# Kernel optimization log

Measured on AMD Instinct MI355X. Metric: run time of the kernel, lower is better.

The kernel has to match this reference:

```python
import jax, jax.numpy as jnp
import numpy as np

C = 128   # d_pair, fixed by the fp8 tri-mul kernel assert
H = 128   # d_hidden


def layer_norm(x, w, b, eps=1e-5):
    m = jnp.mean(x, axis=-1, keepdims=True)
    v = jnp.mean(jnp.square(x - m), axis=-1, keepdims=True)
    return (x - m) * jax.lax.rsqrt(v + eps) * w + b


def setup_inputs() -> dict:
    key = jax.random.key(0)
    ks = jax.random.split(key, 12)
    B, N = 1, 512
    s_in = 1.0 / np.sqrt(C)
    s_h = 1.0 / np.sqrt(H)
    return {
        "z": jax.random.normal(ks[0], (B, N, N, C), jnp.float32),
        "mask": jnp.ones((B, N, N), jnp.float32),
        "ln_in_w": jnp.ones((C,), jnp.float32),
        "ln_in_b": jnp.zeros((C,), jnp.float32),
        "w_ap": jax.random.normal(ks[1], (C, H), jnp.float32) * s_in,
        "b_ap": jnp.zeros((H,), jnp.float32),
        "w_ag": jax.random.normal(ks[2], (C, H), jnp.float32) * s_in,
        "b_ag": jnp.zeros((H,), jnp.float32),
        "w_bp": jax.random.normal(ks[3], (C, H), jnp.float32) * s_in,
        "b_bp": jnp.zeros((H,), jnp.float32),
        "w_bg": jax.random.normal(ks[4], (C, H), jnp.float32) * s_in,
        "b_bg": jnp.zeros((H,), jnp.float32),
        "ln_out_w": jnp.ones((H,), jnp.float32),
        "ln_out_b": jnp.zeros((H,), jnp.float32),
        "w_o": jax.random.normal(ks[5], (H, C), jnp.float32) * s_h,
        "b_o": jnp.zeros((C,), jnp.float32),
        "w_g": jax.random.normal(ks[6], (C, C), jnp.float32) * s_in,
        "b_g": jnp.zeros((C,), jnp.float32),
    }


def reference(z, mask, ln_in_w, ln_in_b, w_ap, b_ap, w_ag, b_ag,
              w_bp, b_bp, w_bg, b_bg, ln_out_w, ln_out_b, w_o, b_o, w_g, b_g):
    # Triangular multiplicative update (outgoing), gated projections.
    z_ln = layer_norm(z, ln_in_w, ln_in_b)                      # [B,N,N,C]
    m = mask[..., None]                                         # [B,N,N,1]
    a = m * jax.nn.sigmoid(z_ln @ w_ag + b_ag) * (z_ln @ w_ap + b_ap)
    b = m * jax.nn.sigmoid(z_ln @ w_bg + b_bg) * (z_ln @ w_bp + b_bp)
    # outgoing: x[b,i,j,c] = sum_k a[b,i,k,c] * b[b,j,k,c]
    x = jnp.einsum("bikc,bjkc->bijc", a, b)                     # [B,N,N,H]
    x = layer_norm(x, ln_out_w, ln_out_b)
    g = jax.nn.sigmoid(z_ln @ w_g + b_g)                        # output gate
    return g * (x @ w_o + b_o)
```

## Files before the change

kernel.cpp:

```cpp
#include <hip/hip_runtime.h>
#include <hip/hip_bf16.h>
#include <stdint.h>

#define NDIM 512
#define NN (NDIM*NDIM)
#define CDIM 128
#define LDSP 136

typedef __attribute__((ext_vector_type(8))) short short8;
typedef __attribute__((ext_vector_type(4))) short short4v;
typedef __attribute__((ext_vector_type(4))) float f32x4;
typedef unsigned long long ull;

__device__ __forceinline__ unsigned short f2bf(float f) {
    union { float f; uint32_t u; } v; v.f = f;
    uint32_t u = v.u;
    return (unsigned short)((u + 0x7FFFu + ((u >> 16) & 1u)) >> 16);
}
__device__ __forceinline__ float bf2f(unsigned short b) {
    union { uint32_t u; float f; } v; v.u = ((uint32_t)b) << 16;
    return v.f;
}
__device__ __forceinline__ f32x4 mfma16(short8 a, short8 b, f32x4 c) {
    return __builtin_amdgcn_mfma_f32_16x16x32_bf16(a, b, c, 0, 0, 0);
}
__device__ __forceinline__ void gl_lds16(const void* g, void* l) {
    __builtin_amdgcn_global_load_lds((const __attribute__((address_space(1))) void*)g,
                                     (__attribute__((address_space(3))) void*)l,
                                     16, 0, 0);
}

__global__ void k0_prep(const float* __restrict__ w_ag, const float* __restrict__ w_ap,
                        const float* __restrict__ w_bg, const float* __restrict__ w_bp,
                        const float* __restrict__ w_g,  const float* __restrict__ w_o,
                        unsigned short* __restrict__ Wfrag, unsigned short* __restrict__ Wo_t)
{
    int idx = blockIdx.x * 256 + threadIdx.x;
    if (idx < 10240) {
        int lane = idx & 63;
        int n  = (idx >> 6) & 3;
        int kk = (idx >> 8) & 3;
        int h  = (idx >> 10) & 1;
        int s  = idx >> 11;
        const float* w = (s==0) ? w_ag : (s==1) ? w_ap : (s==2) ? w_bg : (s==3) ? w_bp : w_g;
        int col = h*64 + n*16 + (lane & 15);
        int k0  = kk*32 + (lane >> 4)*8;
        short8 pk;
        #pragma unroll
        for (int e = 0; e < 8; e++)
            pk[e] = (short)f2bf(w[(k0 + e)*128 + col]);
        *(short8*)(Wfrag + (size_t)idx*8) = pk;
    } else if (idx < 10240 + 16384) {
        int i2 = idx - 10240;
        int cc = i2 >> 7, hh = i2 & 127;
        Wo_t[i2] = f2bf(w_o[hh*128 + cc]);
    }
}

__global__ __launch_bounds__(256, 2) void k1_proj(
    const float* __restrict__ z, const float* __restrict__ mask,
    const float* __restrict__ lnw, const float* __restrict__ lnb,
    const unsigned short* __restrict__ Wfrag,
    const float* __restrict__ b_ag, const float* __restrict__ b_ap,
    const float* __restrict__ b_bg, const float* __restrict__ b_bp,
    const float* __restrict__ b_g,
    unsigned short* __restrict__ a_t, unsigned short* __restrict__ b_t,
    unsigned short* __restrict__ g_out)
{
    __shared__ unsigned short zb[128*LDSP];
    __shared__ float mask_s[128];
    __shared__ float lnw_s[128];
    __shared__ float lnb_s[128];
    __shared__ float bias_s[640];

    const int t = threadIdx.x;
    const int pos0 = blockIdx.x * 128;
    const int tid2 = t >> 1, half = t & 1;
    const int wave = t >> 6, lane = t & 63;
    const int lr = lane & 15, lh = lane >> 4;

    if (t < 128) {
        lnw_s[t] = lnw[t];
        lnb_s[t] = lnb[t];
        mask_s[t] = mask[pos0 + t];
    }
    for (int i = t; i < 640; i += 256) {
        int s = i >> 7, c = i & 127;
        const float* bp = (s==0) ? b_ag : (s==1) ? b_ap : (s==2) ? b_bg : (s==3) ? b_bp : b_g;
        bias_s[i] = bp[c];
    }

    float v[64];
    float s0 = 0.f, s1 = 0.f;
    {
        const float* zr = z + (size_t)(pos0 + tid2) * CDIM + half * 64;
        #pragma unroll
        for (int i = 0; i < 16; i++) {
            float4 q = *(const float4*)(zr + i*4);
            v[i*4+0] = q.x; v[i*4+1] = q.y; v[i*4+2] = q.z; v[i*4+3] = q.w;
        }
        #pragma unroll
        for (int i = 0; i < 64; i++) { s0 += v[i]; s1 += v[i]*v[i]; }
        s0 += __shfl_xor(s0, 1);
        s1 += __shfl_xor(s1, 1);
    }
    __syncthreads();
    {
        float m  = s0 * (1.f/128.f);
        float va = s1 * (1.f/128.f) - m*m;
        float rs = rsqrtf(va + 1e-5f);
        #pragma unroll
        for (int i = 0; i < 8; i++) {
            short8 pk;
            #pragma unroll
            for (int j = 0; j < 8; j++) {
                int c = half*64 + i*8 + j;
                pk[j] = (short)f2bf((v[i*8+j]-m)*rs*lnw_s[c] + lnb_s[c]);
            }
            *(short8*)&zb[tid2*LDSP + half*64 + i*8] = pk;
        }
    }
    __syncthreads();

    const int rowA0 = (wave*32 + lr)*LDSP;
    const int rowA1 = (wave*32 + 16 + lr)*LDSP;
    const unsigned short* wfl = Wfrag + (size_t)lane*8;

    auto gemmh = [&](int s, int h, f32x4 (&acc)[2][4]) {
        const unsigned short* wf = wfl + (size_t)(s*2 + h)*8192;
        short8 wbuf[16];
        #pragma unroll
        for (int i = 0; i < 16; i++)
            wbuf[i] = *(const short8*)(wf + i*512);
        #pragma unroll
        for (int m = 0; m < 2; m++)
            #pragma unroll
            for (int n = 0; n < 4; n++) { f32x4 zz = {0.f,0.f,0.f,0.f}; acc[m][n] = zz; }
        #pragma unroll
        for (int kk = 0; kk < 4; kk++) {
            const int k0 = kk*32 + lh*8;
            short8 af0 = *(const short8*)&zb[rowA0 + k0];
            short8 af1 = *(const short8*)&zb[rowA1 + k0];
            #pragma unroll
            for (int n = 0; n < 4; n++) {
                acc[0][n] = mfma16(af0, wbuf[kk*4 + n], acc[0][n]);
                acc[1][n] = mfma16(af1, wbuf[kk*4 + n], acc[1][n]);
            }
        }
    };

    auto pair_half = [&](int sG, int sP, int h, unsigned short* dstg) {
        f32x4 G[2][4], P[2][4];
        gemmh(sG, h, G);
        gemmh(sP, h, P);
        const int odd = lh & 1;
        const int base = wave*32 + lh*4 + (odd ? 12 : 0);
        #pragma unroll
        for (int n = 0; n < 4; n++) {
            int col = h*64 + n*16 + lr;
            float bgv = bias_s[sG*128 + col];
            float bpv = bias_s[sP*128 + col];
            union { short4v v; ull u; } p0, p1;
            #pragma unroll
            for (int r = 0; r < 4; r++) {
                float g0 = 1.f / (1.f + __expf(-(G[0][n][r] + bgv)));
                p0.v[r] = (short)f2bf(mask_s[wave*32 + lh*4 + r] * g0 * (P[0][n][r] + bpv));
                float g1 = 1.f / (1.f + __expf(-(G[1][n][r] + bgv)));
                p1.v[r] = (short)f2bf(mask_s[wave*32 + 16 + lh*4 + r] * g1 * (P[1][n][r] + bpv));
            }
            ull r0 = __shfl_xor(p0.u, 16);
            ull r1 = __shfl_xor(p1.u, 16);
            union { ull u[2]; short8 v; } outv;
            outv.u[0] = odd ? r1 : p0.u;
            outv.u[1] = odd ? p1.u : r0;
            *(short8*)(dstg + (size_t)col*NN + pos0 + base) = outv.v;
        }
    };

    pair_half(0, 1, 0, a_t);
    pair_half(0, 1, 1, a_t);
    pair_half(2, 3, 0, b_t);
    pair_half(2, 3, 1, b_t);

    f32x4 G0[2][4], G1[2][4];
    gemmh(4, 0, G0);
    gemmh(4, 1, G1);
    __syncthreads();
    #pragma unroll
    for (int m = 0; m < 2; m++) {
        int rb = wave*32 + m*16 + lh*4;
        #pragma unroll
        for (int n = 0; n < 4; n++) {
            int c0 = n*16 + lr;
            int c1 = 64 + n*16 + lr;
            float b0 = bias_s[512 + c0];
            float b1 = bias_s[512 + c1];
            #pragma unroll
            for (int r = 0; r < 4; r++) {
                zb[(rb + r)*LDSP + c0] = f2bf(1.f / (1.f + __expf(-(G0[m][n][r] + b0))));
                zb[(rb + r)*LDSP + c1] = f2bf(1.f / (1.f + __expf(-(G1[m][n][r] + b1))));
            }
        }
    }
    __syncthreads();
    {
        const unsigned short* src = zb + tid2*LDSP + half*64;
        unsigned short* dst = g_out + (size_t)(pos0 + tid2)*CDIM + half*64;
        #pragma unroll
        for (int i = 0; i < 8; i++)
            *(short8*)(dst + i*8) = *(const short8*)(src + i*8);
    }
}

__global__ __launch_bounds__(256, 2) void k2_einsum(
    const unsigned short* __restrict__ a_t,
    const unsigned short* __restrict__ b_t,
    unsigned short* __restrict__ x_t)
{
    __shared__ unsigned short As[128*64];
    __shared__ unsigned short Bs[128*64];

    const int c  = blockIdx.y;
    const int ti = (blockIdx.x >> 2) * 128;
    const int tj = (blockIdx.x & 3) * 128;
    const int t = threadIdx.x;
    const int wave = t >> 6, lane = t & 63;
    const int lr = lane & 15, lh = lane >> 4;
    const int wm = wave >> 1, wn = wave & 1;

    const unsigned short* Ag = a_t + (size_t)c*NN + (size_t)ti*NDIM;
    const unsigned short* Bg = b_t + (size_t)c*NN + (size_t)tj*NDIM;

    const int srow = wave*32 + (lane >> 3);
    const int scol = (lane & 7) * 8;

    f32x4 acc[4][4] = {};

    for (int k0 = 0; k0 < NDIM; k0 += 64) {
        __syncthreads();
        #pragma unroll
        for (int it = 0; it < 4; it++) {
            int r = srow + it*8;
            gl_lds16(Ag + (size_t)r*NDIM + k0 + scol, (void*)(As + (wave*32 + it*8)*64));
            gl_lds16(Bg + (size_t)r*NDIM + k0 + scol, (void*)(Bs + (wave*32 + it*8)*64));
        }
        asm volatile("s_waitcnt vmcnt(0)" ::: "memory");
        __syncthreads();
        #pragma unroll
        for (int kk = 0; kk < 2; kk++) {
            const int kof = kk*32 + lh*8;
            short8 af[4], bfr[4];
            #pragma unroll
            for (int m = 0; m < 4; m++)
                af[m] = *(const short8*)&As[(wm*64 + m*16 + lr)*64 + kof];
            #pragma unroll
            for (int n = 0; n < 4; n++)
                bfr[n] = *(const short8*)&Bs[(wn*64 + n*16 + lr)*64 + kof];
            #pragma unroll
            for (int m = 0; m < 4; m++)
                #pragma unroll
                for (int n = 0; n < 4; n++)
                    acc[m][n] = mfma16(af[m], bfr[n], acc[m][n]);
        }
    }

    #pragma unroll
    for (int m = 0; m < 4; m++) {
        int row = ti + wm*64 + m*16 + lh*4;
        #pragma unroll
        for (int n = 0; n < 4; n++) {
            int col = tj + wn*64 + n*16 + lr;
            unsigned short* dst = x_t + (size_t)c*NN + (size_t)row*NDIM + col;
            #pragma unroll
            for (int r = 0; r < 4; r++)
                dst[(size_t)r*NDIM] = f2bf(acc[m][n][r]);
        }
    }
}

__global__ __launch_bounds__(256, 2) void k3_out(
    const unsigned short* __restrict__ x_t,
    const unsigned short* __restrict__ g_in,
    const unsigned short* __restrict__ Wo_t,
    const float* __restrict__ lnw, const float* __restrict__ lnb,
    const float* __restrict__ b_o,
    float* __restrict__ out)
{
    __shared__ unsigned short xb[128*LDSP];
    __shared__ unsigned short zl[128*LDSP];
    __shared__ float lnw_s[128];
    __shared__ float lnb_s[128];
    __shared__ float bo_s[128];

    const int t = threadIdx.x;
    const int pos0 = blockIdx.x * 128;
    const int tid2 = t >> 1, half = t & 1;
    const int wave = t >> 6, lane = t & 63;
    const int lr = lane & 15, lh = lane >> 4;

    if (t < 128) { lnw_s[t] = lnw[t]; lnb_s[t] = lnb[t]; bo_s[t] = b_o[t]; }

    {
        const unsigned short* src = x_t + (size_t)tid2*NN + pos0 + half*64;
        unsigned short* dst = xb + tid2*LDSP + half*64;
        #pragma unroll
        for (int i = 0; i < 8; i++)
            *(short8*)(dst + i*8) = *(const short8*)(src + i*8);
    }
    __syncthreads();

    {
        float v[64];
        float s0 = 0.f, s1 = 0.f;
        #pragma unroll
        for (int i = 0; i < 64; i++) {
            float x = bf2f(xb[(half*64 + i)*LDSP + tid2]);
            v[i] = x; s0 += x; s1 += x*x;
        }
        s0 += __shfl_xor(s0, 1);
        s1 += __shfl_xor(s1, 1);
        float m  = s0 * (1.f/128.f);
        float va = s1 * (1.f/128.f) - m*m;
        float rs = rsqrtf(va + 1e-5f);
        #pragma unroll
        for (int i = 0; i < 64; i++) {
            int cc = half*64 + i;
            zl[tid2*LDSP + cc] = f2bf((v[i]-m)*rs*lnw_s[cc] + lnb_s[cc]);
        }
    }
    __syncthreads();

    {
        const unsigned short* src = Wo_t + ((size_t)tid2*128 + half*64);
        unsigned short* dst = xb + tid2*LDSP + half*64;
        #pragma unroll
        for (int i = 0; i < 8; i++)
            *(short8*)(dst + i*8) = *(const short8*)(src + i*8);
    }
    __syncthreads();

    f32x4 acc[2][8];
    #pragma unroll
    for (int m = 0; m < 2; m++)
        #pragma unroll
        for (int n = 0; n < 8; n++) { f32x4 zz = {0.f,0.f,0.f,0.f}; acc[m][n] = zz; }

    #pragma unroll
    for (int kk = 0; kk < 4; kk++) {
        const int k0 = kk*32 + lh*8;
        short8 af0 = *(const short8*)&zl[(wave*32 + lr)*LDSP + k0];
        short8 af1 = *(const short8*)&zl[(wave*32 + 16 + lr)*LDSP + k0];
        #pragma unroll
        for (int n = 0; n < 8; n++) {
            short8 bf = *(const short8*)&xb[(n*16 + lr)*LDSP + k0];
            acc[0][n] = mfma16(af0, bf, acc[0][n]);
            acc[1][n] = mfma16(af1, bf, acc[1][n]);
        }
    }
    __syncthreads();

    {
        const unsigned short* src = g_in + (size_t)(pos0 + tid2)*CDIM + half*64;
        unsigned short* dst = zl + tid2*LDSP + half*64;
        #pragma unroll
        for (int i = 0; i < 8; i++)
            *(short8*)(dst + i*8) = *(const short8*)(src + i*8);
    }
    __syncthreads();

    #pragma unroll
    for (int m = 0; m < 2; m++) {
        int rb = wave*32 + m*16 + lh*4;
        #pragma unroll
        for (int n = 0; n < 8; n++) {
            int col = n*16 + lr;
            float bo = bo_s[col];
            #pragma unroll
            for (int r = 0; r < 4; r++) {
                int row = rb + r;
                float gv = bf2f(zl[row*LDSP + col]);
                out[(size_t)(pos0 + row)*CDIM + col] = gv * (acc[m][n][r] + bo);
            }
        }
    }
}

extern "C" void kernel_launch(void* const* d_in, const int* in_sizes, int n_in,
                              void* d_out, int out_size, void* d_ws, size_t ws_size,
                              hipStream_t stream) {
    const float* z        = (const float*)d_in[0];
    const float* mask     = (const float*)d_in[1];
    const float* ln_in_w  = (const float*)d_in[2];
    const float* ln_in_b  = (const float*)d_in[3];
    const float* w_ap     = (const float*)d_in[4];
    const float* b_ap     = (const float*)d_in[5];
    const float* w_ag     = (const float*)d_in[6];
    const float* b_ag     = (const float*)d_in[7];
    const float* w_bp     = (const float*)d_in[8];
    const float* b_bp     = (const float*)d_in[9];
    const float* w_bg     = (const float*)d_in[10];
    const float* b_bg     = (const float*)d_in[11];
    const float* ln_out_w = (const float*)d_in[12];
    const float* ln_out_b = (const float*)d_in[13];
    const float* w_o      = (const float*)d_in[14];
    const float* b_o      = (const float*)d_in[15];
    const float* w_g      = (const float*)d_in[16];
    const float* b_g      = (const float*)d_in[17];

    char* ws = (char*)d_ws;
    const size_t BUF = (size_t)NN * 128 * 2;
    unsigned short* a_t   = (unsigned short*)(ws);
    unsigned short* b_t   = (unsigned short*)(ws + BUF);
    unsigned short* g_b   = (unsigned short*)(ws + 2*BUF);
    unsigned short* x_t   = (unsigned short*)(ws + 3*BUF);
    unsigned short* Wfrag = (unsigned short*)(ws + 4*BUF);
    unsigned short* Wo_t  = (unsigned short*)(ws + 4*BUF + (size_t)10240*8*2);

    k0_prep<<<104, 256, 0, stream>>>(w_ag, w_ap, w_bg, w_bp, w_g, w_o, Wfrag, Wo_t);
    k1_proj<<<NN/128, 256, 0, stream>>>(z, mask, ln_in_w, ln_in_b, Wfrag,
                                        b_ag, b_ap, b_bg, b_bp, b_g, a_t, b_t, g_b);
    k2_einsum<<<dim3(16, 128), 256, 0, stream>>>(a_t, b_t, x_t);
    k3_out<<<NN/128, 256, 0, stream>>>(x_t, g_b, Wo_t, ln_out_w, ln_out_b, b_o,
                                       (float*)d_out);
}
```

Baseline: 307.4 us.

## Switch intermediates to fp16 and split k1 projections across 8 waves

```diff
diff --git a/kernel.cpp b/kernel.cpp
--- a/kernel.cpp
+++ b/kernel.cpp
@@ -10,19 +10,22 @@
 typedef __attribute__((ext_vector_type(8))) short short8;
 typedef __attribute__((ext_vector_type(4))) short short4v;
 typedef __attribute__((ext_vector_type(4))) float f32x4;
+typedef __attribute__((ext_vector_type(8))) _Float16 half8;
 typedef unsigned long long ull;
 
-__device__ __forceinline__ unsigned short f2bf(float f) {
-    union { float f; uint32_t u; } v; v.f = f;
-    uint32_t u = v.u;
-    return (unsigned short)((u + 0x7FFFu + ((u >> 16) & 1u)) >> 16);
-}
-__device__ __forceinline__ float bf2f(unsigned short b) {
-    union { uint32_t u; float f; } v; v.u = ((uint32_t)b) << 16;
-    return v.f;
+__device__ __forceinline__ unsigned short f2h(float f) {
+    union { _Float16 h; unsigned short u; } v;
+    v.h = (_Float16)f;
+    return v.u;
+}
+__device__ __forceinline__ float h2f(unsigned short u) {
+    union { _Float16 h; unsigned short u; } v;
+    v.u = u;
+    return (float)v.h;
 }
 __device__ __forceinline__ f32x4 mfma16(short8 a, short8 b, f32x4 c) {
-    return __builtin_amdgcn_mfma_f32_16x16x32_bf16(a, b, c, 0, 0, 0);
+    return __builtin_amdgcn_mfma_f32_16x16x32_f16(
+        __builtin_bit_cast(half8, a), __builtin_bit_cast(half8, b), c, 0, 0, 0);
 }
 __device__ __forceinline__ void gl_lds16(const void* g, void* l) {
     __builtin_amdgcn_global_load_lds((const __attribute__((address_space(1))) void*)g,
@@ -48,16 +51,16 @@
         short8 pk;
         #pragma unroll
         for (int e = 0; e < 8; e++)
-            pk[e] = (short)f2bf(w[(k0 + e)*128 + col]);
+            pk[e] = (short)f2h(w[(k0 + e)*128 + col]);
         *(short8*)(Wfrag + (size_t)idx*8) = pk;
     } else if (idx < 10240 + 16384) {
         int i2 = idx - 10240;
         int cc = i2 >> 7, hh = i2 & 127;
-        Wo_t[i2] = f2bf(w_o[hh*128 + cc]);
-    }
-}
-
-__global__ __launch_bounds__(256, 2) void k1_proj(
+        Wo_t[i2] = f2h(w_o[hh*128 + cc]);
+    }
+}
+
+__global__ __launch_bounds__(512, 4) void k1_proj(
     const float* __restrict__ z, const float* __restrict__ mask,
     const float* __restrict__ lnw, const float* __restrict__ lnb,
     const unsigned short* __restrict__ Wfrag,
@@ -75,8 +78,9 @@
 
     const int t = threadIdx.x;
     const int pos0 = blockIdx.x * 128;
-    const int tid2 = t >> 1, half = t & 1;
+    const int row4 = t >> 2, q = t & 3;
     const int wave = t >> 6, lane = t & 63;
+    const int wl = wave & 3, wg = wave >> 2;
     const int lr = lane & 15, lh = lane >> 4;
 
     if (t < 128) {
@@ -84,25 +88,27 @@
         lnb_s[t] = lnb[t];
         mask_s[t] = mask[pos0 + t];
     }
-    for (int i = t; i < 640; i += 256) {
+    for (int i = t; i < 640; i += 512) {
         int s = i >> 7, c = i & 127;
         const float* bp = (s==0) ? b_ag : (s==1) ? b_ap : (s==2) ? b_bg : (s==3) ? b_bp : b_g;
         bias_s[i] = bp[c];
     }
 
-    float v[64];
+    float v[32];
     float s0 = 0.f, s1 = 0.f;
     {
-        const float* zr = z + (size_t)(pos0 + tid2) * CDIM + half * 64;
-        #pragma unroll
-        for (int i = 0; i < 16; i++) {
-            float4 q = *(const float4*)(zr + i*4);
-            v[i*4+0] = q.x; v[i*4+1] = q.y; v[i*4+2] = q.z; v[i*4+3] = q.w;
-        }
-        #pragma unroll
-        for (int i = 0; i < 64; i++) { s0 += v[i]; s1 += v[i]*v[i]; }
+        const float* zr = z + (size_t)(pos0 + row4) * CDIM + q * 32;
+        #pragma unroll
+        for (int i = 0; i < 8; i++) {
+            float4 qv = *(const float4*)(zr + i*4);
+            v[i*4+0] = qv.x; v[i*4+1] = qv.y; v[i*4+2] = qv.z; v[i*4+3] = qv.w;
+        }
+        #pragma unroll
+        for (int i = 0; i < 32; i++) { s0 += v[i]; s1 += v[i]*v[i]; }
         s0 += __shfl_xor(s0, 1);
         s1 += __shfl_xor(s1, 1);
+        s0 += __shfl_xor(s0, 2);
+        s1 += __shfl_xor(s1, 2);
     }
     __syncthreads();
     {
@@ -110,20 +116,20 @@
         float va = s1 * (1.f/128.f) - m*m;
         float rs = rsqrtf(va + 1e-5f);
         #pragma unroll
-        for (int i = 0; i < 8; i++) {
+        for (int i = 0; i < 4; i++) {
             short8 pk;
             #pragma unroll
             for (int j = 0; j < 8; j++) {
-                int c = half*64 + i*8 + j;
-                pk[j] = (short)f2bf((v[i*8+j]-m)*rs*lnw_s[c] + lnb_s[c]);
+                int c = q*32 + i*8 + j;
+                pk[j] = (short)f2h((v[i*8+j]-m)*rs*lnw_s[c] + lnb_s[c]);
             }
-            *(short8*)&zb[tid2*LDSP + half*64 + i*8] = pk;
-        }
-    }
-    __syncthreads();
-
-    const int rowA0 = (wave*32 + lr)*LDSP;
-    const int rowA1 = (wave*32 + 16 + lr)*LDSP;
+            *(short8*)&zb[row4*LDSP + q*32 + i*8] = pk;
+        }
+    }
+    __syncthreads();
+
+    const int rowA0 = (wl*32 + lr)*LDSP;
+    const int rowA1 = (wl*32 + 16 + lr)*LDSP;
     const unsigned short* wfl = Wfrag + (size_t)lane*8;
 
     auto gemmh = [&](int s, int h, f32x4 (&acc)[2][4]) {
@@ -154,7 +160,7 @@
         gemmh(sG, h, G);
         gemmh(sP, h, P);
         const int odd = lh & 1;
-        const int base = wave*32 + lh*4 + (odd ? 12 : 0);
+        const int base = wl*32 + lh*4 + (odd ? 12 : 0);
         #pragma unroll
         for (int n = 0; n < 4; n++) {
             int col = h*64 + n*16 + lr;
@@ -164,9 +170,9 @@
             #pragma unroll
             for (int r = 0; r < 4; r++) {
                 float g0 = 1.f / (1.f + __expf(-(G[0][n][r] + bgv)));
-                p0.v[r] = (short)f2bf(mask_s[wave*32 + lh*4 + r] * g0 * (P[0][n][r] + bpv));
+                p0.v[r] = (short)f2h(mask_s[wl*32 + lh*4 + r] * g0 * (P[0][n][r] + bpv));
                 float g1 = 1.f / (1.f + __expf(-(G[1][n][r] + bgv)));
-                p1.v[r] = (short)f2bf(mask_s[wave*32 + 16 + lh*4 + r] * g1 * (P[1][n][r] + bpv));
+                p1.v[r] = (short)f2h(mask_s[wl*32 + 16 + lh*4 + r] * g1 * (P[1][n][r] + bpv));
             }
             ull r0 = __shfl_xor(p0.u, 16);
             ull r1 = __shfl_xor(p1.u, 16);
@@ -177,37 +183,35 @@
         }
     };
 
-    pair_half(0, 1, 0, a_t);
-    pair_half(0, 1, 1, a_t);
-    pair_half(2, 3, 0, b_t);
-    pair_half(2, 3, 1, b_t);
-
-    f32x4 G0[2][4], G1[2][4];
-    gemmh(4, 0, G0);
-    gemmh(4, 1, G1);
+    if (wg == 0) {
+        pair_half(0, 1, 0, a_t);
+        pair_half(0, 1, 1, a_t);
+    } else {
+        pair_half(2, 3, 0, b_t);
+        pair_half(2, 3, 1, b_t);
+    }
+
+    f32x4 G[2][4];
+    gemmh(4, wg, G);
     __syncthreads();
     #pragma unroll
     for (int m = 0; m < 2; m++) {
-        int rb = wave*32 + m*16 + lh*4;
+        int rb = wl*32 + m*16 + lh*4;
         #pragma unroll
         for (int n = 0; n < 4; n++) {
-            int c0 = n*16 + lr;
-            int c1 = 64 + n*16 + lr;
+            int c0 = wg*64 + n*16 + lr;
             float b0 = bias_s[512 + c0];
-            float b1 = bias_s[512 + c1];
-            #pragma unroll
-            for (int r = 0; r < 4; r++) {
-                zb[(rb + r)*LDSP + c0] = f2bf(1.f / (1.f + __expf(-(G0[m][n][r] + b0))));
-                zb[(rb + r)*LDSP + c1] = f2bf(1.f / (1.f + __expf(-(G1[m][n][r] + b1))));
-            }
-        }
-    }
-    __syncthreads();
-    {
-        const unsigned short* src = zb + tid2*LDSP + half*64;
-        unsigned short* dst = g_out + (size_t)(pos0 + tid2)*CDIM + half*64;
-        #pragma unroll
-        for (int i = 0; i < 8; i++)
+            #pragma unroll
+            for (int r = 0; r < 4; r++)
+                zb[(rb + r)*LDSP + c0] = f2h(1.f / (1.f + __expf(-(G[m][n][r] + b0))));
+        }
+    }
+    __syncthreads();
+    {
+        const unsigned short* src = zb + row4*LDSP + q*32;
+        unsigned short* dst = g_out + (size_t)(pos0 + row4)*CDIM + q*32;
+        #pragma unroll
+        for (int i = 0; i < 4; i++)
             *(short8*)(dst + i*8) = *(const short8*)(src + i*8);
     }
 }
@@ -273,7 +277,7 @@
             unsigned short* dst = x_t + (size_t)c*NN + (size_t)row*NDIM + col;
             #pragma unroll
             for (int r = 0; r < 4; r++)
-                dst[(size_t)r*NDIM] = f2bf(acc[m][n][r]);
+                dst[(size_t)r*NDIM] = f2h(acc[m][n][r]);
         }
     }
 }
@@ -314,7 +318,7 @@
         float s0 = 0.f, s1 = 0.f;
         #pragma unroll
         for (int i = 0; i < 64; i++) {
-            float x = bf2f(xb[(half*64 + i)*LDSP + tid2]);
+            float x = h2f(xb[(half*64 + i)*LDSP + tid2]);
             v[i] = x; s0 += x; s1 += x*x;
         }
         s0 += __shfl_xor(s0, 1);
@@ -325,7 +329,7 @@
         #pragma unroll
         for (int i = 0; i < 64; i++) {
             int cc = half*64 + i;
-            zl[tid2*LDSP + cc] = f2bf((v[i]-m)*rs*lnw_s[cc] + lnb_s[cc]);
+            zl[tid2*LDSP + cc] = f2h((v[i]-m)*rs*lnw_s[cc] + lnb_s[cc]);
         }
     }
     __syncthreads();
@@ -378,7 +382,7 @@
             #pragma unroll
             for (int r = 0; r < 4; r++) {
                 int row = rb + r;
-                float gv = bf2f(zl[row*LDSP + col]);
+                float gv = h2f(zl[row*LDSP + col]);
                 out[(size_t)(pos0 + row)*CDIM + col] = gv * (acc[m][n][r] + bo);
             }
         }
@@ -417,7 +421,7 @@
     unsigned short* Wo_t  = (unsigned short*)(ws + 4*BUF + (size_t)10240*8*2);
 
     k0_prep<<<104, 256, 0, stream>>>(w_ag, w_ap, w_bg, w_bp, w_g, w_o, Wfrag, Wo_t);
-    k1_proj<<<NN/128, 256, 0, stream>>>(z, mask, ln_in_w, ln_in_b, Wfrag,
+    k1_proj<<<NN/128, 512, 0, stream>>>(z, mask, ln_in_w, ln_in_b, Wfrag,
                                         b_ag, b_ap, b_bg, b_bp, b_g, a_t, b_t, g_b);
     k2_einsum<<<dim3(16, 128), 256, 0, stream>>>(a_t, b_t, x_t);
     k3_out<<<NN/128, 256, 0, stream>>>(x_t, g_b, Wo_t, ln_out_w, ln_out_b, b_o,
```

New measurement: 423.3 us. 37.7% more time.
